# Performance work log

Hardware: AMD Instinct MI355X
Metric: run time of the kernel (lower is better)

Reference implementation:

```python
import jax, jax.numpy as jnp
import numpy as np

D, N = 512, 256          # transition steps, batch
H, L, V = 128, 64, 32000 # h_dim, label_dim, lexicon_size


def _valid_transitions(seed=0):
    # generate a valid shift/reduce schedule: reduce only when stack depth >= 2
    rng = np.random.default_rng(seed)
    ptr = np.zeros(N, np.int64)
    trans = np.zeros((D, N), np.int32)
    for t in range(D):
        r = ((rng.random(N) < 0.6) & (ptr >= 2)).astype(np.int32)
        trans[t] = r
        ptr += 1 - 2 * r  # every step pushes 1; reduce pops 2 first
    return jnp.asarray(trans)


def setup_inputs() -> dict:
    key = jax.random.key(0)
    k1, k2, k3 = jax.random.split(key, 3)
    transitions = _valid_transitions()
    labels_idx = jax.random.randint(k1, (D, N), 0, V, dtype=jnp.int32)
    emb = jax.random.normal(k2, (V, L), jnp.float32) * 0.02
    emb = emb.at[0].set(0.0)  # padding_idx=0
    arg_dim = L + 2 * H
    W = jax.random.normal(k3, (arg_dim, 5 * H), jnp.float32) / np.sqrt(arg_dim).astype(np.float32)
    b = jnp.zeros((5 * H,), jnp.float32)
    leaf = jnp.zeros((H,), jnp.float32)  # leaf_input placeholder vector
    return {"transitions": transitions, "labels_idx": labels_idx,
            "emb": emb, "W": W, "b": b, "leaf": leaf}


def _cell(x, hl, hr, cl, cr, W, b):
    # binary TreeLSTM (Tai et al.): gates from concat(label, h_left, h_right)
    g = jnp.concatenate([x, hl, hr], axis=-1) @ W + b  # [N, 5H]
    i, fl, fr, o, u = jnp.split(g, 5, axis=-1)
    c = jax.nn.sigmoid(i) * jnp.tanh(u) + jax.nn.sigmoid(fl) * cl + jax.nn.sigmoid(fr) * cr
    h = jax.nn.sigmoid(o) * jnp.tanh(c)
    return c, h


def reference(transitions, labels_idx, emb, W, b, leaf):
    labels = emb[labels_idx]  # [D,N,L]
    bidx = jnp.arange(N)

    def step(carry, inp):
        h_st, c_st, idx_st, ptr = carry  # [D,N,H],[D,N,H],[D,N],[N]
        t, mask, lab = inp
        mf = mask.astype(bool)[:, None]
        # right popped first, then left (matches _get_indices call order)
        ridx = idx_st[(ptr - 1) % D, bidx]
        lidx = idx_st[(ptr - 2) % D, bidx]
        hl = jnp.where(mf, h_st[lidx, bidx], leaf)
        hr = jnp.where(mf, h_st[ridx, bidx], leaf)
        cl = jnp.where(mf, c_st[lidx, bidx], leaf)
        cr = jnp.where(mf, c_st[ridx, bidx], leaf)
        c, h = _cell(lab, hl, hr, cl, cr, W, b)
        h_st = h_st.at[t].set(h)   # embeddings_stack[step] = h
        c_st = c_st.at[t].set(c)   # cells_stack[step] = c
        newptr = ptr - 2 * mask    # pops (if reduce)
        idx_st = idx_st.at[newptr, bidx].set(t)  # push current step for all batch
        return (h_st, c_st, idx_st, newptr + 1), None

    h_st = jnp.zeros((D, N, H), jnp.float32)
    c_st = jnp.zeros((D, N, H), jnp.float32)
    idx_st = jnp.zeros((D, N), jnp.int32)
    ptr = jnp.zeros((N,), jnp.int32)
    (h_st, c_st, _, _), _ = jax.lax.scan(
        step, (h_st, c_st, idx_st, ptr),
        (jnp.arange(D, dtype=jnp.int32), transitions, labels))
    # original returns (thin_stack[1][D-1], thin_stack[0][D-1]) = (cells, embeddings)
    return c_st[D - 1], h_st[D - 1]
```

## Files before the change

kernel.cpp:

```cpp
#include <hip/hip_runtime.h>
#include <stdint.h>


#define D     512
#define HD    128
#define LD    64
#define NTHR  512
#define GPR   328

typedef unsigned long long u64t;

__device__ __forceinline__ float sigf(float x){ return 1.0f/(1.0f+__expf(-x)); }
__device__ __forceinline__ float tanh_(float x){ return 1.0f-2.0f/(__expf(2.0f*x)+1.0f); }
__device__ __forceinline__ u64t gld64(const float* p){
  return __hip_atomic_load((const u64t*)p, __ATOMIC_RELAXED, __HIP_MEMORY_SCOPE_AGENT);
}
__device__ __forceinline__ u64t gld64r(const u64t* p){
  return __hip_atomic_load(p, __ATOMIC_RELAXED, __HIP_MEMORY_SCOPE_AGENT);
}
__device__ __forceinline__ void gst32(float* p, float v){
  __hip_atomic_store(p, v, __ATOMIC_RELAXED, __HIP_MEMORY_SCOPE_AGENT);
}
__device__ __forceinline__ void gst64r(u64t* p, u64t v){
  __hip_atomic_store(p, v, __ATOMIC_RELAXED, __HIP_MEMORY_SCOPE_AGENT);
}
__device__ __forceinline__ u64t packw(float v, unsigned tg){
  return ((u64t)tg << 32) | (u64t)__float_as_uint(v);
}
__device__ __forceinline__ float loww(u64t w){
  return __uint_as_float((unsigned)(w & 0xffffffffu));
}

__global__ __launch_bounds__(NTHR,2) void spinn_kernel(
    const int* __restrict__ trans, const int* __restrict__ labels,
    const float* __restrict__ emb, const float* __restrict__ W,
    const float* __restrict__ bias, const float* __restrict__ leaf,
    float* __restrict__ out, u64t* __restrict__ ring,
    float* __restrict__ rec, float* __restrict__ cown)
{
  const int bid = blockIdx.x;
  const int g2 = ((bid>>4)<<3) | (bid&7);
  const int sl = (bid>>3)&1, ps = sl^1;
  const int gb0 = g2*2;
  const int tid = threadIdx.x;
  const int kg = tid>>6, lane = tid&63;
  const int cq = lane;

  __shared__ __align__(16) float xs[2][2][320];
  __shared__ __align__(16) float gpq[16][GPR];
  __shared__ float bsl[320];
  __shared__ float lshd[HD];
  __shared__ float clb[2][2][64];
  __shared__ uint8_t mS[D][2];
  __shared__ short liA[D][2];
  __shared__ unsigned short stk_[2][D];

  float4 wr4[40]; float wr1[40];
  {
    const int gq = (cq>>4)*128 + sl*64 + ((cq*4)&63);
    const int gu = 512 + sl*64 + cq;
#pragma unroll
    for (int j=0;j<40;++j){
      int k = kg*40 + j;
      wr4[j] = *(const float4*)(W + (size_t)k*640 + gq);
      wr1[j] = W[(size_t)k*640 + gu];
    }
  }
  if (tid < 320){
    int c = tid;
    int gc = (c < 256) ? ((c>>6)*128 + sl*64 + (c&63)) : (512 + sl*64 + (c-256));
    bsl[c] = bias[gc];
  }
  if (tid < HD) lshd[tid] = leaf[tid];
  if (tid < 2){
    int b = tid, p = 0;
    for (int t=0;t<D;++t){
      int m = trans[t*256 + gb0 + b];
      short li = 0;
      if (m) li = (short)stk_[b][p-2];
      mS[t][b] = (uint8_t)m; liA[t][b] = li;
      int np = p - 2*m; stk_[b][np] = (unsigned short)t; p = np+1;
    }
  }
  __syncthreads();

  for (int idx = tid; idx < 640; idx += NTHR){
    int b = (idx >= 320) ? 1 : 0;
    int r = idx - b*320;
    if (r < 64){
      int row = labels[gb0 + b];
      xs[0][b][r] = emb[(size_t)row*LD + r];
    } else {
      xs[0][b][r] = lshd[(r-64)&127];
    }
  }
  __syncthreads();

  auto gemm = [&](int cur){
    float4 a0 = {0.f,0.f,0.f,0.f}, a1 = {0.f,0.f,0.f,0.f};
    float u0 = 0.f, u1 = 0.f;
#pragma unroll
    for (int j4=0;j4<10;++j4){
      int k = kg*40 + j4*4;
      float4 x0 = *(const float4*)&xs[cur][0][k];
      float4 x1 = *(const float4*)&xs[cur][1][k];
      float xa0[4] = {x0.x,x0.y,x0.z,x0.w};
      float xa1[4] = {x1.x,x1.y,x1.z,x1.w};
#pragma unroll
      for (int jj=0;jj<4;++jj){
        float4 w = wr4[j4*4+jj];
        float wu = wr1[j4*4+jj];
        a0.x = __builtin_fmaf(w.x, xa0[jj], a0.x);
        a0.y = __builtin_fmaf(w.y, xa0[jj], a0.y);
        a0.z = __builtin_fmaf(w.z, xa0[jj], a0.z);
        a0.w = __builtin_fmaf(w.w, xa0[jj], a0.w);
        a1.x = __builtin_fmaf(w.x, xa1[jj], a1.x);
        a1.y = __builtin_fmaf(w.y, xa1[jj], a1.y);
        a1.z = __builtin_fmaf(w.z, xa1[jj], a1.z);
        a1.w = __builtin_fmaf(w.w, xa1[jj], a1.w);
        u0 = __builtin_fmaf(wu, xa0[jj], u0);
        u1 = __builtin_fmaf(wu, xa1[jj], u1);
      }
    }
    *(float4*)&gpq[kg*2+0][cq*4] = a0;
    *(float4*)&gpq[kg*2+1][cq*4] = a1;
    gpq[kg*2+0][256+cq] = u0;
    gpq[kg*2+1][256+cq] = u1;
  };

  float ccprev = 0.f;

  for (int t=0;t<D;++t){
    const int cur = t&1, nxt = cur^1;

    gemm(cur);
    __syncthreads();

    if (tid < 128){
      const int b = tid>>6, dl = tid&63, gd = sl*64+dl;
      const int m = mS[t][b];
      float s[5];
#pragma unroll
      for (int g=0; g<5; ++g){
        int c = (g<4) ? (g*64+dl) : (256+dl);
        float a = 0.f;
#pragma unroll
        for (int kk=0; kk<8; ++kk) a += gpq[kk*2+b][c];
        s[g] = a + bsl[c];
      }
      float cl_ = m ? clb[cur][b][dl] : lshd[gd];
      float cr_ = m ? ccprev : lshd[gd];
      float cc = sigf(s[0])*tanh_(s[4]) + sigf(s[1])*cl_ + sigf(s[2])*cr_;
      float hh = sigf(s[3])*tanh_(cc);
      ccprev = cc;
      gst64r(ring + (((size_t)(t&7)*128 + g2)*2 + sl)*128 + tid,
             packw(hh, (unsigned)(t+1)));
      size_t ro = (((size_t)t*128 + g2)*2 + sl)*128 + b*64 + dl;
      gst32(rec + ro, hh);
      gst32(cown + ro, cc);
      if (t == D-1){
        out[(size_t)(gb0+b)*HD + gd] = cc;
        out[(size_t)256*HD + (size_t)(gb0+b)*HD + gd] = hh;
      } else {
        xs[nxt][b][192+gd] = mS[t+1][b] ? hh : lshd[gd];
      }
      if (t+2 < D && mS[t+2][b] && liA[t+2][b] == t){
        xs[cur][b][64+gd]  = hh;
        clb[cur][b][dl]    = cc;
      }
    } else if (kg == 2){
      if (t+1 < D){
        int b = lane>>5, jj = lane&31;
        int row = labels[(t+1)*256 + gb0 + b];
        float2 ev = *(const float2*)(emb + (size_t)row*LD + jj*2);
        xs[nxt][b][jj*2]   = ev.x;
        xs[nxt][b][jj*2+1] = ev.y;
      }
    } else if (kg == 3){
      if (t+1 < D){
        int b = lane>>5, jj = lane&31;
        int m1 = mS[t+1][b]; int li = liA[t+1][b];
        if (m1){
          if (li <= t-2){
            size_t ro = (((size_t)li*128+g2)*2 + sl)*128 + b*64 + jj*2;
            union{u64t u; float f[2];} h_, c_;
            h_.u = gld64(rec + ro);
            c_.u = gld64(cown + ro);
            xs[nxt][b][64+sl*64+jj*2]   = h_.f[0];
            xs[nxt][b][64+sl*64+jj*2+1] = h_.f[1];
            clb[nxt][b][jj*2]   = c_.f[0];
            clb[nxt][b][jj*2+1] = c_.f[1];
          }
        } else {
          xs[nxt][b][64+sl*64+jj*2]   = lshd[sl*64+jj*2];
          xs[nxt][b][64+sl*64+jj*2+1] = lshd[sl*64+jj*2+1];
          clb[nxt][b][jj*2]   = lshd[sl*64+jj*2];
          clb[nxt][b][jj*2+1] = lshd[sl*64+jj*2+1];
        }
      }
    } else if (kg == 6){
      if (t+1 < D){
        int b = lane>>5, jj = lane&31;
        int m1 = mS[t+1][b]; int li = liA[t+1][b];
        if (m1){
          if (li <= t-2){
            size_t ro = (((size_t)li*128+g2)*2 + ps)*128 + b*64 + jj*2;
            union{u64t u; float f[2];} h_;
            h_.u = gld64(rec + ro);
            xs[nxt][b][64+ps*64+jj*2]   = h_.f[0];
            xs[nxt][b][64+ps*64+jj*2+1] = h_.f[1];
          } else {
            const u64t* rp = ring + (((size_t)((t-1)&7)*128 + g2)*2 + ps)*128
                             + b*64 + jj*2;
            xs[nxt][b][64+ps*64+jj*2]   = loww(gld64r(rp));
            xs[nxt][b][64+ps*64+jj*2+1] = loww(gld64r(rp+1));
          }
        } else {
          xs[nxt][b][64+ps*64+jj*2]   = lshd[ps*64+jj*2];
          xs[nxt][b][64+ps*64+jj*2+1] = lshd[ps*64+jj*2+1];
        }
      }
    } else if (kg == 7){
      if (t+1 < D){
        const u64t* rp = ring + (((size_t)(t&7)*128 + g2)*2 + ps)*128 + lane*2;
        const unsigned want = (unsigned)(t+1);
        u64t w0 = 0, w1 = 0; int it = 0;
        for (;;){
          w0 = gld64r(rp); w1 = gld64r(rp+1);
          int ok = ((unsigned)(w0>>32) == want) & ((unsigned)(w1>>32) == want);
          if (__all(ok)) break;
          if (it >= 4) __builtin_amdgcn_s_sleep(1);
          if (++it > (1<<20)) break;
        }
        int b = lane>>5, jj = lane&31;
        if (mS[t+1][b]){
          xs[nxt][b][192+ps*64+jj*2]   = loww(w0);
          xs[nxt][b][192+ps*64+jj*2+1] = loww(w1);
        } else {
          xs[nxt][b][192+ps*64+jj*2]   = lshd[ps*64+jj*2];
          xs[nxt][b][192+ps*64+jj*2+1] = lshd[ps*64+jj*2+1];
        }
      }
    }
    __syncthreads();
  }
}

extern "C" void kernel_launch(void* const* d_in, const int* in_sizes, int n_in,
                              void* d_out, int out_size, void* d_ws, size_t ws_size,
                              hipStream_t stream) {
  (void)in_sizes; (void)n_in; (void)out_size; (void)ws_size;
  const int*   trans  = (const int*)d_in[0];
  const int*   labels = (const int*)d_in[1];
  const float* emb    = (const float*)d_in[2];
  const float* W      = (const float*)d_in[3];
  const float* bias   = (const float*)d_in[4];
  const float* leaf   = (const float*)d_in[5];
  float* out = (float*)d_out;

  uint8_t* ws = (uint8_t*)d_ws;
  u64t*  ring = (u64t*)ws;
  float* rec  = (float*)(ws + ((size_t)8<<20));
  float* cown = (float*)(ws + ((size_t)72<<20));

  spinn_kernel<<<dim3(256), dim3(NTHR), 0, stream>>>(
      trans, labels, emb, W, bias, leaf, out, ring, rec, cown);
}
```

Measured before the change: 1.836 ms.

## Exchange partial gate sums between block pairs instead of hidden-state halves

Each block in a pair now publishes its 640 partial gate pre-activations through a tagged mailbox. Both blocks then redundantly compute the full 128-wide cell update for both batch rows, so neither has to wait on or reload the partner's half of h through the ring and rec buffers. Only slice 0 writes rec/cown, and the reduce-operand loads now fetch full 128-wide rows from a single place. The cost is more global traffic per step (640 tagged words each way) and a spin-wait placed directly on the critical path before the cell math, rather than one overlapped with the next-step prefetch.

```diff
diff --git a/kernel.cpp b/kernel.cpp
--- a/kernel.cpp
+++ b/kernel.cpp
@@ -35,7 +35,7 @@
     const int* __restrict__ trans, const int* __restrict__ labels,
     const float* __restrict__ emb, const float* __restrict__ W,
     const float* __restrict__ bias, const float* __restrict__ leaf,
-    float* __restrict__ out, u64t* __restrict__ ring,
+    float* __restrict__ out, u64t* __restrict__ mail,
     float* __restrict__ rec, float* __restrict__ cown)
 {
   const int bid = blockIdx.x;
@@ -48,9 +48,9 @@
 
   __shared__ __align__(16) float xs[2][2][320];
   __shared__ __align__(16) float gpq[16][GPR];
-  __shared__ float bsl[320];
+  __shared__ float bsl[640];
   __shared__ float lshd[HD];
-  __shared__ float clb[2][2][64];
+  __shared__ float clb[2][2][HD];
   __shared__ uint8_t mS[D][2];
   __shared__ short liA[D][2];
   __shared__ unsigned short stk_[2][D];
@@ -66,11 +66,7 @@
       wr1[j] = W[(size_t)k*640 + gu];
     }
   }
-  if (tid < 320){
-    int c = tid;
-    int gc = (c < 256) ? ((c>>6)*128 + sl*64 + (c&63)) : (512 + sl*64 + (c-256));
-    bsl[c] = bias[gc];
-  }
+  for (int c = tid; c < 640; c += NTHR) bsl[c] = bias[c];
   if (tid < HD) lshd[tid] = leaf[tid];
   if (tid < 2){
     int b = tid, p = 0;
@@ -136,110 +132,114 @@
     gemm(cur);
     __syncthreads();
 
-    if (tid < 128){
-      const int b = tid>>6, dl = tid&63, gd = sl*64+dl;
+    {
+      u64t* mo = mail + (((size_t)(t&3)*128 + g2)*2 + sl)*640;
+      {
+        const int w = tid;
+        const int b = (w >= 320), c = w - b*320;
+        float a = 0.f;
+#pragma unroll
+        for (int kk=0; kk<8; ++kk) a += gpq[kk*2+b][c];
+        gst64r(mo + w, packw(a, (unsigned)(t+1)));
+      }
+      if (tid < 128){
+        const int w = 512 + tid;
+        const int c = w - 320;
+        float a = 0.f;
+#pragma unroll
+        for (int kk=0; kk<8; ++kk) a += gpq[kk*2+1][c];
+        gst64r(mo + w, packw(a, (unsigned)(t+1)));
+      }
+    }
+
+    if (tid < 256){
+      const int b = tid>>7, h = tid&127, dl = h&63;
+      const int own = ((h>>6) == sl);
       const int m = mS[t][b];
       float s[5];
-#pragma unroll
-      for (int g=0; g<5; ++g){
-        int c = (g<4) ? (g*64+dl) : (256+dl);
-        float a = 0.f;
-#pragma unroll
-        for (int kk=0; kk<8; ++kk) a += gpq[kk*2+b][c];
-        s[g] = a + bsl[c];
-      }
-      float cl_ = m ? clb[cur][b][dl] : lshd[gd];
-      float cr_ = m ? ccprev : lshd[gd];
-      float cc = sigf(s[0])*tanh_(s[4]) + sigf(s[1])*cl_ + sigf(s[2])*cr_;
-      float hh = sigf(s[3])*tanh_(cc);
+      if (own){
+#pragma unroll
+        for (int g=0; g<5; ++g){
+          const int c = (g<4) ? (g*64+dl) : (256+dl);
+          float a = 0.f;
+#pragma unroll
+          for (int kk=0; kk<8; ++kk) a += gpq[kk*2+b][c];
+          s[g] = a;
+        }
+      } else {
+        const u64t* mi = mail + (((size_t)(t&3)*128 + g2)*2 + ps)*640 + b*320;
+        const unsigned want = (unsigned)(t+1);
+        u64t pw[5];
+#pragma unroll
+        for (int g=0;g<4;++g) pw[g] = gld64r(mi + g*64 + dl);
+        pw[4] = gld64r(mi + 256 + dl);
+        int it = 0;
+        while (!__all(((unsigned)(pw[0]>>32) == want) &
+                      ((unsigned)(pw[1]>>32) == want) &
+                      ((unsigned)(pw[2]>>32) == want) &
+                      ((unsigned)(pw[3]>>32) == want) &
+                      ((unsigned)(pw[4]>>32) == want))){
+          if (it >= 4) __builtin_amdgcn_s_sleep(1);
+#pragma unroll
+          for (int g=0;g<4;++g) pw[g] = gld64r(mi + g*64 + dl);
+          pw[4] = gld64r(mi + 256 + dl);
+          if (++it > (1<<17)) break;
+        }
+#pragma unroll
+        for (int g=0;g<5;++g) s[g] = loww(pw[g]);
+      }
+#pragma unroll
+      for (int g=0;g<4;++g) s[g] += bsl[g*128 + h];
+      s[4] += bsl[512 + h];
+
+      const float cl_ = m ? clb[cur][b][h] : lshd[h];
+      const float cr_ = m ? ccprev : lshd[h];
+      const float cc = sigf(s[0])*tanh_(s[4]) + sigf(s[1])*cl_ + sigf(s[2])*cr_;
+      const float hh = sigf(s[3])*tanh_(cc);
       ccprev = cc;
-      gst64r(ring + (((size_t)(t&7)*128 + g2)*2 + sl)*128 + tid,
-             packw(hh, (unsigned)(t+1)));
-      size_t ro = (((size_t)t*128 + g2)*2 + sl)*128 + b*64 + dl;
-      gst32(rec + ro, hh);
-      gst32(cown + ro, cc);
+
+      if (sl == 0){
+        const size_t ro = (((size_t)t*128 + g2)*2 + b)*HD + h;
+        gst32(rec + ro, hh);
+        gst32(cown + ro, cc);
+      }
       if (t == D-1){
-        out[(size_t)(gb0+b)*HD + gd] = cc;
-        out[(size_t)256*HD + (size_t)(gb0+b)*HD + gd] = hh;
+        out[(size_t)(gb0+b)*HD + h] = cc;
+        out[(size_t)256*HD + (size_t)(gb0+b)*HD + h] = hh;
       } else {
-        xs[nxt][b][192+gd] = mS[t+1][b] ? hh : lshd[gd];
+        xs[nxt][b][192+h] = mS[t+1][b] ? hh : lshd[h];
       }
       if (t+2 < D && mS[t+2][b] && liA[t+2][b] == t){
-        xs[cur][b][64+gd]  = hh;
-        clb[cur][b][dl]    = cc;
-      }
-    } else if (kg == 2){
+        xs[cur][b][64+h] = hh;
+        clb[cur][b][h]   = cc;
+      }
+    } else if (tid < 384){
       if (t+1 < D){
-        int b = lane>>5, jj = lane&31;
-        int row = labels[(t+1)*256 + gb0 + b];
-        float2 ev = *(const float2*)(emb + (size_t)row*LD + jj*2);
-        xs[nxt][b][jj*2]   = ev.x;
-        xs[nxt][b][jj*2+1] = ev.y;
-      }
-    } else if (kg == 3){
-      if (t+1 < D){
-        int b = lane>>5, jj = lane&31;
-        int m1 = mS[t+1][b]; int li = liA[t+1][b];
+        const int idx = tid-256, b = idx>>6, jj = idx&63, h2 = jj*2;
+        const int m1 = mS[t+1][b]; const int li = liA[t+1][b];
         if (m1){
           if (li <= t-2){
-            size_t ro = (((size_t)li*128+g2)*2 + sl)*128 + b*64 + jj*2;
+            const size_t ro = (((size_t)li*128 + g2)*2 + b)*HD + h2;
             union{u64t u; float f[2];} h_, c_;
             h_.u = gld64(rec + ro);
             c_.u = gld64(cown + ro);
-            xs[nxt][b][64+sl*64+jj*2]   = h_.f[0];
-            xs[nxt][b][64+sl*64+jj*2+1] = h_.f[1];
-            clb[nxt][b][jj*2]   = c_.f[0];
-            clb[nxt][b][jj*2+1] = c_.f[1];
+            xs[nxt][b][64+h2]   = h_.f[0];
+            xs[nxt][b][64+h2+1] = h_.f[1];
+            clb[nxt][b][h2]     = c_.f[0];
+            clb[nxt][b][h2+1]   = c_.f[1];
           }
         } else {
-          xs[nxt][b][64+sl*64+jj*2]   = lshd[sl*64+jj*2];
-          xs[nxt][b][64+sl*64+jj*2+1] = lshd[sl*64+jj*2+1];
-          clb[nxt][b][jj*2]   = lshd[sl*64+jj*2];
-          clb[nxt][b][jj*2+1] = lshd[sl*64+jj*2+1];
+          xs[nxt][b][64+h2]   = lshd[h2];
+          xs[nxt][b][64+h2+1] = lshd[h2+1];
+          clb[nxt][b][h2]     = lshd[h2];
+          clb[nxt][b][h2+1]   = lshd[h2+1];
         }
       }
-    } else if (kg == 6){
+    } else {
       if (t+1 < D){
-        int b = lane>>5, jj = lane&31;
-        int m1 = mS[t+1][b]; int li = liA[t+1][b];
-        if (m1){
-          if (li <= t-2){
-            size_t ro = (((size_t)li*128+g2)*2 + ps)*128 + b*64 + jj*2;
-            union{u64t u; float f[2];} h_;
-            h_.u = gld64(rec + ro);
-            xs[nxt][b][64+ps*64+jj*2]   = h_.f[0];
-            xs[nxt][b][64+ps*64+jj*2+1] = h_.f[1];
-          } else {
-            const u64t* rp = ring + (((size_t)((t-1)&7)*128 + g2)*2 + ps)*128
-                             + b*64 + jj*2;
-            xs[nxt][b][64+ps*64+jj*2]   = loww(gld64r(rp));
-            xs[nxt][b][64+ps*64+jj*2+1] = loww(gld64r(rp+1));
-          }
-        } else {
-          xs[nxt][b][64+ps*64+jj*2]   = lshd[ps*64+jj*2];
-          xs[nxt][b][64+ps*64+jj*2+1] = lshd[ps*64+jj*2+1];
-        }
-      }
-    } else if (kg == 7){
-      if (t+1 < D){
-        const u64t* rp = ring + (((size_t)(t&7)*128 + g2)*2 + ps)*128 + lane*2;
-        const unsigned want = (unsigned)(t+1);
-        u64t w0 = 0, w1 = 0; int it = 0;
-        for (;;){
-          w0 = gld64r(rp); w1 = gld64r(rp+1);
-          int ok = ((unsigned)(w0>>32) == want) & ((unsigned)(w1>>32) == want);
-          if (__all(ok)) break;
-          if (it >= 4) __builtin_amdgcn_s_sleep(1);
-          if (++it > (1<<20)) break;
-        }
-        int b = lane>>5, jj = lane&31;
-        if (mS[t+1][b]){
-          xs[nxt][b][192+ps*64+jj*2]   = loww(w0);
-          xs[nxt][b][192+ps*64+jj*2+1] = loww(w1);
-        } else {
-          xs[nxt][b][192+ps*64+jj*2]   = lshd[ps*64+jj*2];
-          xs[nxt][b][192+ps*64+jj*2+1] = lshd[ps*64+jj*2+1];
-        }
+        const int idx = tid-384, b = idx>>6, jj = idx&63;
+        const int row = labels[(t+1)*256 + gb0 + b];
+        xs[nxt][b][jj] = emb[(size_t)row*LD + jj];
       }
     }
     __syncthreads();
@@ -259,10 +259,10 @@
   float* out = (float*)d_out;
 
   uint8_t* ws = (uint8_t*)d_ws;
-  u64t*  ring = (u64t*)ws;
+  u64t*  mail = (u64t*)ws;
   float* rec  = (float*)(ws + ((size_t)8<<20));
   float* cown = (float*)(ws + ((size_t)72<<20));
 
   spinn_kernel<<<dim3(256), dim3(NTHR), 0, stream>>>(
-      trans, labels, emb, W, bias, leaf, out, ring, rec, cown);
-}
+      trans, labels, emb, W, bias, leaf, out, mail, rec, cown);
+}
```

New measurement: 1.710 ms. 1.07x faster.
